# Kernel optimization log

Measured on AMD Instinct MI355X. Metric: run time of the kernel, lower is better.

## Reference

```python
import jax, jax.numpy as jnp
import numpy as np

B, S, FEAT = 64, 196, 512
D_MODEL, D_INPUT = 1024, 512
HEADS = 8          # cross-attention heads
SYNC_HEADS = 8     # neuron-sync attention heads (num_attn_heads)
ITERS = 50         # thought ticks
MEM = 25           # memory_length
NLM_H = 16         # memory_hidden_dims
OUT = 1000         # out_dims


def _n(key, i, shape, scale=0.02):
    return scale * jax.random.normal(jax.random.fold_in(key, i), shape, dtype=jnp.float32)


def setup_inputs() -> dict:
    key = jax.random.key(0)
    return {
        "x": jax.random.normal(jax.random.fold_in(key, 0), (B, S, FEAT), dtype=jnp.float32),
        "kv_w": _n(key, 1, (D_INPUT, FEAT)), "kv_b": jnp.zeros((D_INPUT,), jnp.float32),
        "ln_kv_s": jnp.ones((D_INPUT,), jnp.float32), "ln_kv_b": jnp.zeros((D_INPUT,), jnp.float32),
        "q_w": _n(key, 2, (D_INPUT, D_MODEL)), "q_b": jnp.zeros((D_INPUT,), jnp.float32),
        "in_proj_w": _n(key, 3, (3 * D_INPUT, D_INPUT)), "in_proj_b": jnp.zeros((3 * D_INPUT,), jnp.float32),
        "out_proj_w": _n(key, 4, (D_INPUT, D_INPUT)), "out_proj_b": jnp.zeros((D_INPUT,), jnp.float32),
        "W_q": _n(key, 5, (D_MODEL, D_MODEL), 0.03), "W_k": _n(key, 6, (D_MODEL, D_MODEL), 0.03),
        "W_v": _n(key, 7, (D_MODEL, D_MODEL), 0.03),
        "syn_w": _n(key, 8, (2 * D_MODEL, D_INPUT + D_MODEL)), "syn_b": jnp.zeros((2 * D_MODEL,), jnp.float32),
        "syn_ln_s": jnp.ones((D_MODEL,), jnp.float32), "syn_ln_b": jnp.zeros((D_MODEL,), jnp.float32),
        "nlm_w1": _n(key, 9, (MEM, 2 * NLM_H, D_MODEL), 0.1), "nlm_b1": jnp.zeros((D_MODEL, 2 * NLM_H), jnp.float32),
        "nlm_w2": _n(key, 10, (NLM_H, 2, D_MODEL), 0.1), "nlm_b2": jnp.zeros((D_MODEL, 2), jnp.float32),
        "start_activated_state": _n(key, 11, (D_MODEL,), 0.03),
        "start_trace": _n(key, 12, (D_MODEL, MEM), 0.03),
        "out_w": _n(key, 13, (OUT, D_MODEL)), "out_b": jnp.zeros((OUT,), jnp.float32),
    }


def _ln(x, s, b, eps=1e-5):
    m = x.mean(-1, keepdims=True)
    v = x.var(-1, keepdims=True)
    return (x - m) / jnp.sqrt(v + eps) * s + b


def _glu(x):
    a, g = jnp.split(x, 2, axis=-1)
    return a * jax.nn.sigmoid(g)


def reference(x, kv_w, kv_b, ln_kv_s, ln_kv_b, q_w, q_b, in_proj_w, in_proj_b,
              out_proj_w, out_proj_b, W_q, W_k, W_v, syn_w, syn_b, syn_ln_s, syn_ln_b,
              nlm_w1, nlm_b1, nlm_w2, nlm_b2, start_activated_state, start_trace,
              out_w, out_b):
    b = x.shape[0]
    dh_sync = D_MODEL // SYNC_HEADS
    dh = D_INPUT // HEADS

    # kv_proj: Linear + LayerNorm over backbone features (backbone='none')
    kv = _ln(x @ kv_w.T + kv_b, ln_kv_s, ln_kv_b)  # (B,S,Di)
    wq_c, wk_c, wv_c = jnp.split(in_proj_w, 3, axis=0)
    bq_c, bk_c, bv_c = jnp.split(in_proj_b, 3, axis=0)
    Kc = (kv @ wk_c.T + bk_c).reshape(b, S, HEADS, dh).transpose(0, 2, 1, 3)  # (B,H,S,dh)
    Vc = (kv @ wv_c.T + bv_c).reshape(b, S, HEADS, dh).transpose(0, 2, 1, 3)

    def sync_attn(hist, cur):
        # hist: (B,D,T) post-activation history; cur: (B,D) current post-activations
        hr = jnp.swapaxes(hist, 1, 2)  # (B,T,D)
        T = hr.shape[1]
        Q = (hr @ W_q.T).reshape(b, T, SYNC_HEADS, dh_sync).transpose(0, 2, 1, 3)  # (B,H,T,dh)
        K = (hr @ W_k.T).reshape(b, T, SYNC_HEADS, dh_sync).transpose(0, 2, 1, 3)
        V = (cur @ W_v.T).reshape(b, SYNC_HEADS, dh_sync)  # (B,H,dh)
        # neuron-vs-neuron scores: (B,H,dh,dh)
        scores = jnp.einsum('bhtd,bhte->bhde', Q, K) / jnp.sqrt(jnp.float32(dh_sync))
        w = jax.nn.softmax(scores, axis=-1)
        att = jnp.einsum('bhde,bhe->bhd', w, V)  # (B,H,dh)
        # torch: attended.transpose(1,2).reshape(B, D)
        return att.transpose(0, 2, 1).reshape(b, D_MODEL)

    def cross_attn(sync_a):
        q = sync_a @ q_w.T + q_b  # (B,Di)
        Qh = (q @ wq_c.T + bq_c).reshape(b, HEADS, 1, dh)
        s = jnp.einsum('bhqd,bhkd->bhqk', Qh, Kc) / jnp.sqrt(jnp.float32(dh))
        w = jax.nn.softmax(s, axis=-1)
        o = jnp.einsum('bhqk,bhkd->bhqd', w, Vc).transpose(0, 2, 1, 3).reshape(b, D_INPUT)
        return o @ out_proj_w.T + out_proj_b

    state_trace0 = jnp.broadcast_to(start_trace[None], (b, D_MODEL, MEM))
    act0 = jnp.broadcast_to(start_activated_state[None], (b, D_MODEL))
    hist0 = jnp.broadcast_to(start_activated_state[None, :, None], (b, D_MODEL, MEM))
    log_nc = jnp.log(jnp.float32(OUT))

    def tick(carry, _):
        st, act, hist = carry
        sync_a = sync_attn(hist, act)                     # action synchronisation
        ao = cross_attn(sync_a)                           # (B,Di)
        pre = jnp.concatenate([ao, act], axis=-1)
        state = _ln(_glu(pre @ syn_w.T + syn_b), syn_ln_s, syn_ln_b)  # synapse MLP (depth 1)
        st = jnp.concatenate([st[:, :, 1:], state[:, :, None]], axis=-1)  # sliding pre-act trace
        # per-neuron deep NLM (SuperLinear einsums)
        h = _glu(jnp.einsum('bdm,mhd->bdh', st, nlm_w1) + nlm_b1)
        act_new = _glu(jnp.einsum('bdh,hod->bdo', h, nlm_w2) + nlm_b2)[..., 0]
        hist = jnp.concatenate([hist[:, :, 1:], act_new[:, :, None]], axis=-1)
        sync_o = sync_attn(hist, act_new)                 # output synchronisation
        pred = sync_o @ out_w.T + out_b
        logp = jax.nn.log_softmax(pred, axis=-1)
        ne = -jnp.sum(jnp.exp(logp) * logp, axis=-1) / log_nc
        cert = jnp.stack([ne, 1.0 - ne], axis=-1)
        return (st, act_new, hist), (pred, cert, sync_o)

    _, (preds, certs, syncs) = jax.lax.scan(tick, (state_trace0, act0, hist0), None, length=ITERS)
    predictions = jnp.transpose(preds, (1, 2, 0))  # (B,OUT,T)
    certainties = jnp.transpose(certs, (1, 2, 0))  # (B,2,T)
    return predictions, certainties, syncs[-1]
```

## Files before the change

kernel.cpp:

```cpp
#include <hip/hip_runtime.h>
#include <hip/hip_bf16.h>

typedef __attribute__((ext_vector_type(8))) short short8v;
typedef __attribute__((ext_vector_type(4))) float f32x4;
typedef __attribute__((ext_vector_type(4))) float float4v;

#define DEV __device__ __forceinline__

DEV short f2bfs(float x){
  union { float f; unsigned u; } v; v.f = x;
  unsigned r = (v.u + 0x7FFFu + ((v.u >> 16) & 1u)) >> 16;
  return (short)(unsigned short)r;
}
DEV float bfs2f(short s){
  union { unsigned u; float f; } v; v.u = ((unsigned)(unsigned short)s) << 16;
  return v.f;
}
DEV float sigm(float x){ return 1.f / (1.f + __expf(-x)); }
DEV int zmap(int j){ int g = (j >= 1024) ? 1 : 0; int i = j - (g << 10); return (i & 15) + ((i >> 4) << 5) + (g << 4); }

struct EpiF32 {
  float* C; int ldc;
  DEV void op(const f32x4 (&acc)[4][2], int m0, int n0, int l15, int l4, const float* bias) const {
#pragma unroll
    for (int mi = 0; mi < 4; mi++)
#pragma unroll
      for (int ni = 0; ni < 2; ni++){
        int n = n0 + ni*16 + l15;
        float bb = bias ? bias[n] : 0.f;
#pragma unroll
        for (int r = 0; r < 4; r++){
          int m = m0 + mi*16 + l4*4 + r;
          C[(size_t)m*ldc + n] = acc[mi][ni][r] + bb;
        }
      }
  }
};

struct EpiBF16 {
  short* C; int ldc; int domap;
  DEV void op(const f32x4 (&acc)[4][2], int m0, int n0, int l15, int l4, const float* bias) const {
#pragma unroll
    for (int mi = 0; mi < 4; mi++)
#pragma unroll
      for (int ni = 0; ni < 2; ni++){
        int n = n0 + ni*16 + l15;
        float bb = bias ? bias[n] : 0.f;
#pragma unroll
        for (int r = 0; r < 4; r++){
          int m = m0 + mi*16 + l4*4 + r;
          int mr = domap ? zmap(m) : m;
          C[(size_t)mr*ldc + n] = f2bfs(acc[mi][ni][r] + bb);
        }
      }
  }
};

struct EpiQKV {
  short* Qb; short* Kb; float* vc; int slot;
  DEV void op(const f32x4 (&acc)[4][2], int m0, int n0, int l15, int l4, const float* bias) const {
#pragma unroll
    for (int mi = 0; mi < 4; mi++)
#pragma unroll
      for (int ni = 0; ni < 2; ni++){
        int n = n0 + ni*16 + l15;
#pragma unroll
        for (int r = 0; r < 4; r++){
          int m = m0 + mi*16 + l4*4 + r;
          float v = acc[mi][ni][r];
          if (n < 1024)       Qb[((size_t)m*1024 + n)*32 + slot] = f2bfs(v);
          else if (n < 2048)  Kb[((size_t)m*1024 + (n-1024))*32 + slot] = f2bfs(v);
          else                vc[(size_t)m*1024 + (n-2048)] = v;
        }
      }
  }
};

struct EpiPred {
  float* outp;
  DEV void op(const f32x4 (&acc)[4][2], int m0, int n0, int l15, int l4, const float* bias) const {
#pragma unroll
    for (int mi = 0; mi < 4; mi++)
#pragma unroll
      for (int ni = 0; ni < 2; ni++){
        int n = n0 + ni*16 + l15;
        if (n >= 1000) continue;
        float bb = bias[n];
#pragma unroll
        for (int r = 0; r < 4; r++){
          int m = m0 + mi*16 + l4*4 + r;
          int b = m / 50, tt = m - b*50;
          outp[(size_t)b*50000 + (size_t)n*50 + tt] = acc[mi][ni][r] + bb;
        }
      }
  }
};

struct EpiGlu {
  float* u; float* stats;
  DEV void op(const f32x4 (&acc)[4][2], int m0, int n0, int l15, int l4, const float* bias) const {
    float ba = bias[n0 + l15], bg = bias[n0 + 16 + l15];
    int i = l15 + ((n0 >> 5) << 4);
#pragma unroll
    for (int mi = 0; mi < 4; mi++)
#pragma unroll
      for (int r = 0; r < 4; r++){
        int m = m0 + mi*16 + l4*4 + r;
        float a = acc[mi][0][r] + ba;
        float g = acc[mi][1][r] + bg;
        float uv = a * sigm(g);
        u[(size_t)m*1024 + i] = uv;
        float s = uv, s2 = uv*uv;
#pragma unroll
        for (int off = 1; off < 16; off <<= 1){ s += __shfl_xor(s, off); s2 += __shfl_xor(s2, off); }
        if (l15 == 0){ atomicAdd(&stats[m], s); atomicAdd(&stats[64 + m], s2); }
      }
  }
};

struct EpiKVpre {
  short* C; float* stats;
  DEV void op(const f32x4 (&acc)[4][2], int m0, int n0, int l15, int l4, const float* bias) const {
    float b0 = bias[n0 + l15], b1 = bias[n0 + 16 + l15];
#pragma unroll
    for (int mi = 0; mi < 4; mi++)
#pragma unroll
      for (int r = 0; r < 4; r++){
        int m = m0 + mi*16 + l4*4 + r;
        float v0 = acc[mi][0][r] + b0;
        float v1 = acc[mi][1][r] + b1;
        C[(size_t)m*512 + n0 + l15]      = f2bfs(v0);
        C[(size_t)m*512 + n0 + 16 + l15] = f2bfs(v1);
        float s = v0 + v1, s2 = v0*v0 + v1*v1;
#pragma unroll
        for (int off = 1; off < 16; off <<= 1){ s += __shfl_xor(s, off); s2 += __shfl_xor(s2, off); }
        if (l15 == 0){ atomicAdd(&stats[m*2], s); atomicAdd(&stats[m*2 + 1], s2); }
      }
  }
};

template<bool ABF16, typename EPI>
__global__ __launch_bounds__(256) void gemm_tn(const void* __restrict__ Aptr, int lda,
    const short* __restrict__ Bw, int ldb, const float* __restrict__ bias,
    int K, float* zbuf, int zn, EPI epi)
{
  int tid = threadIdx.x;
  if (zbuf != nullptr && blockIdx.x == 0 && blockIdx.y == 0 && tid < zn) zbuf[tid] = 0.f;
  const int w = tid >> 6, l15 = tid & 15, l4 = (tid >> 4) & 3;
  const int m0 = blockIdx.y * 64;
  const int n0 = blockIdx.x * 128 + w * 32;
  f32x4 acc[4][2];
#pragma unroll
  for (int mi = 0; mi < 4; mi++)
#pragma unroll
    for (int ni = 0; ni < 2; ni++)
      acc[mi][ni] = (f32x4){0.f, 0.f, 0.f, 0.f};
#pragma unroll 4
  for (int kk = 0; kk < K; kk += 32){
    const int ks = kk + l4*8;
    short8v a[4], bfr[2];
#pragma unroll
    for (int mi = 0; mi < 4; mi++){
      const size_t row = (size_t)(m0 + mi*16 + l15);
      if (ABF16){
        a[mi] = *(const short8v*)((const short*)Aptr + row*lda + ks);
      } else {
        const float* ap = (const float*)Aptr + row*lda + ks;
        float4v f0 = *(const float4v*)ap;
        float4v f1 = *(const float4v*)(ap + 4);
        short8v t;
        t[0]=f2bfs(f0[0]); t[1]=f2bfs(f0[1]); t[2]=f2bfs(f0[2]); t[3]=f2bfs(f0[3]);
        t[4]=f2bfs(f1[0]); t[5]=f2bfs(f1[1]); t[6]=f2bfs(f1[2]); t[7]=f2bfs(f1[3]);
        a[mi] = t;
      }
    }
#pragma unroll
    for (int ni = 0; ni < 2; ni++)
      bfr[ni] = *(const short8v*)(Bw + (size_t)(n0 + ni*16 + l15)*ldb + ks);
#pragma unroll
    for (int mi = 0; mi < 4; mi++)
#pragma unroll
      for (int ni = 0; ni < 2; ni++)
        acc[mi][ni] = __builtin_amdgcn_mfma_f32_16x16x32_bf16(a[mi], bfr[ni], acc[mi][ni], 0, 0, 0);
  }
  epi.op(acc, m0, n0, l15, l4, bias);
}

__global__ __launch_bounds__(256) void cross_attn_k(const float* __restrict__ Qh,
    const short* __restrict__ Kc, const short* __restrict__ Vc, short* __restrict__ oa_bf)
{
  int h = blockIdx.x, b = blockIdx.y, tid = threadIdx.x;
  __shared__ float qs[64];
  __shared__ float wsm[256];
  __shared__ float red[256];
  if (tid < 64) qs[tid] = Qh[b*512 + h*64 + tid];
  __syncthreads();
  float sv = -1e30f;
  if (tid < 196){
    const short* kp = Kc + ((size_t)(b*196 + tid)*512 + h*64);
    float acc = 0.f;
#pragma unroll
    for (int j = 0; j < 64; j += 8){
      short8v kv8 = *(const short8v*)(kp + j);
#pragma unroll
      for (int u8 = 0; u8 < 8; u8++) acc += bfs2f(kv8[u8]) * qs[j + u8];
    }
    sv = acc * 0.125f;
  }
  red[tid] = sv; __syncthreads();
  for (int s = 128; s > 0; s >>= 1){ if (tid < s) red[tid] = fmaxf(red[tid], red[tid + s]); __syncthreads(); }
  float M = red[0]; __syncthreads();
  float e = (tid < 196) ? __expf(sv - M) : 0.f;
  wsm[tid] = e; red[tid] = e; __syncthreads();
  for (int s = 128; s > 0; s >>= 1){ if (tid < s) red[tid] += red[tid + s]; __syncthreads(); }
  float Z = red[0]; __syncthreads();
  int d = tid & 63, c = tid >> 6;
  float acc = 0.f;
  for (int s = c; s < 196; s += 4) acc += wsm[s] * bfs2f(Vc[(size_t)(b*196 + s)*512 + h*64 + d]);
  red[tid] = acc; __syncthreads();
  if (tid < 64){
    float o = (red[tid] + red[tid + 64] + red[tid + 128] + red[tid + 192]) / Z;
    oa_bf[(size_t)b*1536 + h*64 + tid] = f2bfs(o);
  }
}

__global__ __launch_bounds__(256) void nlm_k(const float* __restrict__ u, const float* __restrict__ stats,
    const float* __restrict__ g_s, const float* __restrict__ g_b,
    float* __restrict__ st, const float* __restrict__ w1, const float* __restrict__ b1,
    const float* __restrict__ w2, const float* __restrict__ b2, short* __restrict__ oa_bf, int t)
{
  int tid = threadIdx.x;
  int d_i = tid & 15, b_i = (tid >> 4) & 7, half = tid >> 7;
  int d = blockIdx.x*16 + d_i, b = blockIdx.y*8 + b_i;
  float mu = stats[b] * (1.f/1024.f);
  float var = stats[64 + b] * (1.f/1024.f) - mu*mu;
  float rs = rsqrtf(var + 1e-5f);
  float uv = u[b*1024 + d];
  float state = (uv - mu)*rs*g_s[d] + g_b[d];
  int slot = t % 25;
  if (half == 0) st[((size_t)b*1024 + d)*25 + slot] = state;
  float stv[25];
  int p0 = (t + 1) % 25;
#pragma unroll
  for (int m = 0; m < 25; m++){
    int p = p0 + m; if (p >= 25) p -= 25;
    stv[m] = (p == slot) ? state : st[((size_t)b*1024 + d)*25 + p];
  }
  float pre[16];
#pragma unroll
  for (int hh = 0; hh < 16; hh++) pre[hh] = b1[d*32 + half*16 + hh];
  for (int m = 0; m < 25; m++){
    float sm = stv[m];
#pragma unroll
    for (int hh = 0; hh < 16; hh++) pre[hh] += sm * w1[(size_t)(m*32 + half*16 + hh)*1024 + d];
  }
  __shared__ float pl[2][8][16][16];
#pragma unroll
  for (int hh = 0; hh < 16; hh++) pl[half][b_i][hh][d_i] = pre[hh];
  __syncthreads();
  if (half == 0){
    float p2a = b2[d*2 + 0], p2g = b2[d*2 + 1];
#pragma unroll
    for (int i = 0; i < 16; i++){
      float hv = pl[0][b_i][i][d_i] * sigm(pl[1][b_i][i][d_i]);
      p2a += hv * w2[(size_t)(i*2 + 0)*1024 + d];
      p2g += hv * w2[(size_t)(i*2 + 1)*1024 + d];
    }
    float act = p2a * sigm(p2g);
    oa_bf[(size_t)b*1536 + 512 + d] = f2bfs(act);
  }
}

__global__ __launch_bounds__(256) void sync_attn_k(const short* __restrict__ Qbuf, const short* __restrict__ Kbuf,
    const float* __restrict__ vcur, float* __restrict__ S, short* __restrict__ S_bf,
    short* __restrict__ SyncO, int t)
{
  int h = blockIdx.x, b = blockIdx.y, tid = threadIdx.x;
  __shared__ short8v qlds[512];
  __shared__ short8v klds[512];
  const short* qg = Qbuf + ((size_t)b*1024 + h*128)*32;
  const short* kg = Kbuf + ((size_t)b*1024 + h*128)*32;
#pragma unroll
  for (int it = 0; it < 2; it++){
    int ch = tid + 256*it;
    int d = ch >> 2, c = ch & 3;
    int cs = c ^ ((d >> 1) & 3);
    qlds[d*4 + cs] = *(const short8v*)(qg + d*32 + c*8);
    klds[d*4 + cs] = *(const short8v*)(kg + d*32 + c*8);
  }
  __syncthreads();
  int w = tid >> 6, l15 = tid & 15, l4 = (tid >> 4) & 3;
  short8v af[2], bfr[8];
#pragma unroll
  for (int mi2 = 0; mi2 < 2; mi2++){
    int d = (2*w + mi2)*16 + l15;
    af[mi2] = qlds[d*4 + (l4 ^ ((d >> 1) & 3))];
  }
#pragma unroll
  for (int ni = 0; ni < 8; ni++){
    int e = ni*16 + l15;
    bfr[ni] = klds[e*4 + (l4 ^ ((e >> 1) & 3))];
  }
// ... 15 lines not shown
#pragma unroll
  for (int mi2 = 0; mi2 < 2; mi2++)
#pragma unroll
    for (int r = 0; r < 4; r++){
      float sv[8]; float mx = -1e30f;
#pragma unroll
      for (int ni = 0; ni < 8; ni++){ sv[ni] = acc[mi2][ni][r]*scale; mx = fmaxf(mx, sv[ni]); }
#pragma unroll
      for (int off = 1; off < 16; off <<= 1) mx = fmaxf(mx, __shfl_xor(mx, off));
      float den = 0.f, num = 0.f;
#pragma unroll
      for (int ni = 0; ni < 8; ni++){ float p = __expf(sv[ni] - mx); den += p; num += p*Vv[ni]; }
#pragma unroll
      for (int off = 1; off < 16; off <<= 1){ den += __shfl_xor(den, off); num += __shfl_xor(num, off); }
      if (l15 == 0){
        int d = (2*w + mi2)*16 + l4*4 + r;
        float att = num / den;
        int oi = b*1024 + d*8 + h;
        S[oi] = att;
        S_bf[oi] = f2bfs(att);
        if (t >= 0) SyncO[((size_t)b*50 + t)*1024 + d*8 + h] = f2bfs(att);
      }
    }
}

__global__ __launch_bounds__(256) void vecmat_k(const float* __restrict__ W, int ldw,
    const float* __restrict__ v, const float* __restrict__ add, float* __restrict__ out, int K, int domap)
{
  int w = threadIdx.x >> 6, l = threadIdx.x & 63;
  int n = blockIdx.x*4 + w;
  float s = 0.f;
  for (int k = l; k < K; k += 64) s += W[(size_t)n*ldw + k]*v[k];
#pragma unroll
  for (int off = 32; off; off >>= 1) s += __shfl_xor(s, off);
  if (l == 0){ float o = s + (add ? add[n] : 0.f); out[domap ? zmap(n) : n] = o; }
}

__global__ void castW_k(short* dst, int dld, int drow0, int dcol0,
    const float* src, int sld, int N, int K, int transp, int domap)
{
  size_t idx = (size_t)blockIdx.x*256 + threadIdx.x;
  size_t tot = (size_t)N*K;
  if (idx >= tot) return;
  int n = idx / K, k = idx - (size_t)n*K;
  float vv = 0.f;
  if (src) vv = transp ? src[(size_t)k*sld + n] : src[(size_t)n*sld + k];
// ... 17 lines not shown
  kvp[i] = f2bfs((v - mu)*rsqrtf(var + 1e-5f)*s[c] + bb[c]);
}

__global__ void fill_k(short* Qbuf, short* Kbuf, float* vcur, short* oa_bf,
    float* st, const float* q0, const float* k0, const float* v0,
    const float* start, const float* strace)
{
  size_t i = (size_t)blockIdx.x*256 + threadIdx.x;
  const size_t R0 = 64u*1024u*32u;
  if (i < R0){
    int c = i & 31; int d = (i >> 5) & 1023;
    Qbuf[i] = (c < 25) ? f2bfs(q0[d]) : 0;
    Kbuf[i] = (c < 25) ? f2bfs(k0[d]) : 0;
    return;
  }
  i -= R0;
  if (i < 65536){
    int d = i & 1023; int b = i >> 10;
    vcur[i] = v0[d];
    oa_bf[(size_t)b*1536 + 512 + d] = f2bfs(start[d]);
    return;
  }
  i -= 65536;
  if (i < (size_t)64*1024*25){
    st[i] = strace[i % 25600];
  }
}

__global__ __launch_bounds__(256) void cert_k(const float* __restrict__ preds, float* __restrict__ cert)
{
  int t = blockIdx.x, b = blockIdx.y, tid = threadIdx.x;
  __shared__ float red[256];
  float v[4]; float mx = -1e30f;
#pragma unroll
  for (int i = 0; i < 4; i++){
    int o = tid + i*256;
    v[i] = (o < 1000) ? preds[(size_t)b*50000 + (size_t)o*50 + t] : -1e30f;
    mx = fmaxf(mx, v[i]);
  }
  red[tid] = mx; __syncthreads();
  for (int s = 128; s; s >>= 1){ if (tid < s) red[tid] = fmaxf(red[tid], red[tid + s]); __syncthreads(); }
  float M = red[0]; __syncthreads();
  float z = 0.f, wsum = 0.f;
#pragma unroll
  for (int i = 0; i < 4; i++){
    int o = tid + i*256;
    if (o < 1000){ float p = v[i] - M; float e = __expf(p); z += e; wsum += e*p; }
  }
// ... 52 lines not shown
  auto alloc = [&](size_t bytes)->char*{ char* p = ws + off; off = (off + bytes + 255) & ~(size_t)255; return p; };

  short* qw_B   = (short*)alloc((size_t)1024*512*2);
  short* opw_B  = (short*)alloc((size_t)512*512*2);
  short* Wfq    = (short*)alloc((size_t)512*1024*2);
  float* bfq    = (float*)alloc(512*4);
  short* Wz     = (short*)alloc((size_t)2048*1536*2);
  float* bz     = (float*)alloc(2048*4);
  short* Wqkv   = (short*)alloc((size_t)3072*1024*2);
  short* outwB  = (short*)alloc((size_t)1024*1024*2);
  short* kvw_B  = (short*)alloc((size_t)512*512*2);
  short* wkc_B  = (short*)alloc((size_t)512*512*2);
  short* wvc_B  = (short*)alloc((size_t)512*512*2);
  short* kvp    = (short*)alloc((size_t)12544*512*2);
  float* kvstats= (float*)alloc((size_t)25088*4);
  short* Kc     = (short*)alloc((size_t)12544*512*2);
  short* Vc     = (short*)alloc((size_t)12544*512*2);
  short* Qbuf   = (short*)alloc((size_t)64*1024*32*2);
  short* Kbuf   = (short*)alloc((size_t)64*1024*32*2);
  float* vcur   = (float*)alloc((size_t)65536*4);
  float* S      = (float*)alloc((size_t)65536*4);
  short* S_bf   = (short*)alloc((size_t)65536*2);
  short* SyncO  = (short*)alloc((size_t)64*50*1024*2);
  float* Qh     = (float*)alloc((size_t)32768*4);
  short* oa_bf  = (short*)alloc((size_t)64*1536*2);
  float* ubuf   = (float*)alloc((size_t)65536*4);
  float* stats  = (float*)alloc(128*4);
  float* st     = (float*)alloc((size_t)1638400*4);
  float* q0     = (float*)alloc(1024*4);
  float* k0     = (float*)alloc(1024*4);
  float* v0     = (float*)alloc(1024*4);
  (void)ws_size; (void)in_sizes; (void)n_in; (void)out_size;

  dim3 blk(256);

  castW_k<<<dim3((1024*512+255)/256), blk, 0, stream>>>(qw_B, 512, 0, 0, q_w, 1024, 1024, 512, 1, 0);
  castW_k<<<dim3((512*512+255)/256), blk, 0, stream>>>(opw_B, 512, 0, 0, out_proj_w, 512, 512, 512, 1, 0);
  castW_k<<<dim3((2048*1024+255)/256), blk, 0, stream>>>(Wz, 1536, 0, 512, syn_w + 512, 1536, 2048, 1024, 0, 1);
  castW_k<<<dim3((1024*1024+255)/256), blk, 0, stream>>>(Wqkv, 1024, 0, 0, W_q, 1024, 1024, 1024, 0, 0);
  castW_k<<<dim3((1024*1024+255)/256), blk, 0, stream>>>(Wqkv, 1024, 1024, 0, W_k, 1024, 1024, 1024, 0, 0);
  castW_k<<<dim3((1024*1024+255)/256), blk, 0, stream>>>(Wqkv, 1024, 2048, 0, W_v, 1024, 1024, 1024, 0, 0);
  castW_k<<<dim3((1000*1024+255)/256), blk, 0, stream>>>(outwB, 1024, 0, 0, out_w, 1024, 1000, 1024, 0, 0);
  castW_k<<<dim3((24*1024+255)/256), blk, 0, stream>>>(outwB, 1024, 1000, 0, nullptr, 0, 24, 1024, 0, 0);
  castW_k<<<dim3((512*512+255)/256), blk, 0, stream>>>(kvw_B, 512, 0, 0, kv_w, 512, 512, 512, 0, 0);
  castW_k<<<dim3((512*512+255)/256), blk, 0, stream>>>(wkc_B, 512, 0, 0, in_proj_w + 512*512, 512, 512, 512, 0, 0);
  castW_k<<<dim3((512*512+255)/256), blk, 0, stream>>>(wvc_B, 512, 0, 0, in_proj_w + 1024*512, 512, 512, 512, 0, 0);

  vecmat_k<<<dim3(256), blk, 0, stream>>>(W_q, 1024, start_act, nullptr, q0, 1024, 0);
  vecmat_k<<<dim3(256), blk, 0, stream>>>(W_k, 1024, start_act, nullptr, k0, 1024, 0);
  vecmat_k<<<dim3(256), blk, 0, stream>>>(W_v, 1024, start_act, nullptr, v0, 1024, 0);
  vecmat_k<<<dim3(128), blk, 0, stream>>>(in_proj_w, 512, q_b, in_proj_b, bfq, 512, 0);
  vecmat_k<<<dim3(512), blk, 0, stream>>>(syn_w, 1536, out_proj_b, syn_b, bz, 512, 1);

  gemm_tn<false, EpiBF16><<<dim3(8, 8), blk, 0, stream>>>(in_proj_w, 512, qw_B, 512, nullptr, 512, nullptr, 0, EpiBF16{Wfq, 1024, 0});
  gemm_tn<false, EpiBF16><<<dim3(4, 32), blk, 0, stream>>>(syn_w, 1536, opw_B, 512, nullptr, 512, nullptr, 0, EpiBF16{Wz, 1536, 1});

  zero_k<<<dim3(98), blk, 0, stream>>>(kvstats, 25088);
  gemm_tn<false, EpiKVpre><<<dim3(4, 196), blk, 0, stream>>>(x, 512, kvw_B, 512, kv_b, 512, nullptr, 0, EpiKVpre{kvp, kvstats});
  ln_inplace_k<<<dim3(25088), blk, 0, stream>>>(kvp, kvstats, ln_kv_s, ln_kv_b);
  gemm_tn<true, EpiBF16><<<dim3(4, 196), blk, 0, stream>>>(kvp, 512, wkc_B, 512, in_proj_b + 512, 512, nullptr, 0, EpiBF16{Kc, 512, 0});
  gemm_tn<true, EpiBF16><<<dim3(4, 196), blk, 0, stream>>>(kvp, 512, wvc_B, 512, in_proj_b + 1024, 512, nullptr, 0, EpiBF16{Vc, 512, 0});

  fill_k<<<dim3(14848), blk, 0, stream>>>(Qbuf, Kbuf, vcur, oa_bf, st, q0, k0, v0, start_act, strace);
  sync_attn_k<<<dim3(8, 64), blk, 0, stream>>>(Qbuf, Kbuf, vcur, S, S_bf, SyncO, -1);

  for (int t = 0; t < 50; t++){
    gemm_tn<true, EpiF32><<<dim3(4, 1), blk, 0, stream>>>(S_bf, 1024, Wfq, 1024, bfq, 1024, stats, 128, EpiF32{Qh, 512});
    cross_attn_k<<<dim3(8, 64), blk, 0, stream>>>(Qh, Kc, Vc, oa_bf);
    gemm_tn<true, EpiGlu><<<dim3(16, 1), blk, 0, stream>>>(oa_bf, 1536, Wz, 1536, bz, 1536, nullptr, 0, EpiGlu{ubuf, stats});
    nlm_k<<<dim3(64, 8), blk, 0, stream>>>(ubuf, stats, syn_ln_s, syn_ln_b, st, nlm_w1, nlm_b1, nlm_w2, nlm_b2, oa_bf, t);
    gemm_tn<true, EpiQKV><<<dim3(24, 1), blk, 0, stream>>>(oa_bf + 512, 1536, Wqkv, 1024, nullptr, 1024, nullptr, 0, EpiQKV{Qbuf, Kbuf, vcur, t % 25});
    sync_attn_k<<<dim3(8, 64), blk, 0, stream>>>(Qbuf, Kbuf, vcur, S, S_bf, SyncO, t);
  }

  gemm_tn<true, EpiPred><<<dim3(8, 50), blk, 0, stream>>>(SyncO, 1024, outwB, 1024, out_b, 1024, nullptr, 0, EpiPred{out});
  cert_k<<<dim3(50, 64), blk, 0, stream>>>(out, out + 3200000);
  copy_sync_k<<<dim3(256), blk, 0, stream>>>(S, out + 3206400);
}
```

Measured before the change: 7.639 ms.

## Fuse 50-tick recurrent loop into one persistent kernel with grid barriers

Replaces the roughly 300 per-tick kernel launches with a single persistent cooperative kernel. Its blocks loop over the phases (Q projection fused into cross-attention, GLU GEMM with split-K partials, NLM, QKV GEMM with split-K, sync attention) and separate them with a hand-written atomic grid barrier. The change also moves the state trace to a slot-major layout so NLM reads coalesce. It removes launch overhead and lets the small GEMMs spread over more blocks, at the cost of barrier latency. Correctness depends on every block being co-resident, which the grid size computed from the occupancy query is meant to guarantee.

```diff
diff --git a/kernel.cpp b/kernel.cpp
--- a/kernel.cpp
+++ b/kernel.cpp
@@ -19,181 +19,65 @@
 DEV float sigm(float x){ return 1.f / (1.f + __expf(-x)); }
 DEV int zmap(int j){ int g = (j >= 1024) ? 1 : 0; int i = j - (g << 10); return (i & 15) + ((i >> 4) << 5) + (g << 4); }
 
-struct EpiF32 {
-  float* C; int ldc;
-  DEV void op(const f32x4 (&acc)[4][2], int m0, int n0, int l15, int l4, const float* bias) const {
-#pragma unroll
-    for (int mi = 0; mi < 4; mi++)
-#pragma unroll
-      for (int ni = 0; ni < 2; ni++){
-        int n = n0 + ni*16 + l15;
-        float bb = bias ? bias[n] : 0.f;
-#pragma unroll
-        for (int r = 0; r < 4; r++){
-          int m = m0 + mi*16 + l4*4 + r;
-          C[(size_t)m*ldc + n] = acc[mi][ni][r] + bb;
-        }
-      }
-  }
-};
-
-struct EpiBF16 {
-  short* C; int ldc; int domap;
-  DEV void op(const f32x4 (&acc)[4][2], int m0, int n0, int l15, int l4, const float* bias) const {
-#pragma unroll
-    for (int mi = 0; mi < 4; mi++)
-#pragma unroll
-      for (int ni = 0; ni < 2; ni++){
-        int n = n0 + ni*16 + l15;
-        float bb = bias ? bias[n] : 0.f;
-#pragma unroll
-        for (int r = 0; r < 4; r++){
-          int m = m0 + mi*16 + l4*4 + r;
-          int mr = domap ? zmap(m) : m;
-          C[(size_t)mr*ldc + n] = f2bfs(acc[mi][ni][r] + bb);
-        }
-      }
-  }
-};
-
-struct EpiQKV {
-  short* Qb; short* Kb; float* vc; int slot;
-  DEV void op(const f32x4 (&acc)[4][2], int m0, int n0, int l15, int l4, const float* bias) const {
-#pragma unroll
-    for (int mi = 0; mi < 4; mi++)
-#pragma unroll
-      for (int ni = 0; ni < 2; ni++){
-        int n = n0 + ni*16 + l15;
-#pragma unroll
-        for (int r = 0; r < 4; r++){
-          int m = m0 + mi*16 + l4*4 + r;
-          float v = acc[mi][ni][r];
-          if (n < 1024)       Qb[((size_t)m*1024 + n)*32 + slot] = f2bfs(v);
-          else if (n < 2048)  Kb[((size_t)m*1024 + (n-1024))*32 + slot] = f2bfs(v);
-          else                vc[(size_t)m*1024 + (n-2048)] = v;
-        }
-      }
-  }
-};
-
-struct EpiPred {
-  float* outp;
-  DEV void op(const f32x4 (&acc)[4][2], int m0, int n0, int l15, int l4, const float* bias) const {
-#pragma unroll
-    for (int mi = 0; mi < 4; mi++)
-#pragma unroll
-      for (int ni = 0; ni < 2; ni++){
-        int n = n0 + ni*16 + l15;
-        if (n >= 1000) continue;
-        float bb = bias[n];
-#pragma unroll
-        for (int r = 0; r < 4; r++){
-          int m = m0 + mi*16 + l4*4 + r;
-          int b = m / 50, tt = m - b*50;
-          outp[(size_t)b*50000 + (size_t)n*50 + tt] = acc[mi][ni][r] + bb;
-        }
-      }
-  }
-};
-
-struct EpiGlu {
-  float* u; float* stats;
-  DEV void op(const f32x4 (&acc)[4][2], int m0, int n0, int l15, int l4, const float* bias) const {
-    float ba = bias[n0 + l15], bg = bias[n0 + 16 + l15];
-    int i = l15 + ((n0 >> 5) << 4);
-#pragma unroll
-    for (int mi = 0; mi < 4; mi++)
-#pragma unroll
-      for (int r = 0; r < 4; r++){
-        int m = m0 + mi*16 + l4*4 + r;
-        float a = acc[mi][0][r] + ba;
-        float g = acc[mi][1][r] + bg;
-        float uv = a * sigm(g);
-        u[(size_t)m*1024 + i] = uv;
-        float s = uv, s2 = uv*uv;
-#pragma unroll
-        for (int off = 1; off < 16; off <<= 1){ s += __shfl_xor(s, off); s2 += __shfl_xor(s2, off); }
-        if (l15 == 0){ atomicAdd(&stats[m], s); atomicAdd(&stats[64 + m], s2); }
-      }
-  }
-};
-
-struct EpiKVpre {
-  short* C; float* stats;
-  DEV void op(const f32x4 (&acc)[4][2], int m0, int n0, int l15, int l4, const float* bias) const {
-    float b0 = bias[n0 + l15], b1 = bias[n0 + 16 + l15];
-#pragma unroll
-    for (int mi = 0; mi < 4; mi++)
-#pragma unroll
-      for (int r = 0; r < 4; r++){
-        int m = m0 + mi*16 + l4*4 + r;
-        float v0 = acc[mi][0][r] + b0;
-        float v1 = acc[mi][1][r] + b1;
-        C[(size_t)m*512 + n0 + l15]      = f2bfs(v0);
-        C[(size_t)m*512 + n0 + 16 + l15] = f2bfs(v1);
-        float s = v0 + v1, s2 = v0*v0 + v1*v1;
-#pragma unroll
-        for (int off = 1; off < 16; off <<= 1){ s += __shfl_xor(s, off); s2 += __shfl_xor(s2, off); }
-        if (l15 == 0){ atomicAdd(&stats[m*2], s); atomicAdd(&stats[m*2 + 1], s2); }
-      }
-  }
-};
-
-template<bool ABF16, typename EPI>
-__global__ __launch_bounds__(256) void gemm_tn(const void* __restrict__ Aptr, int lda,
-    const short* __restrict__ Bw, int ldb, const float* __restrict__ bias,
-    int K, float* zbuf, int zn, EPI epi)
-{
-  int tid = threadIdx.x;
-  if (zbuf != nullptr && blockIdx.x == 0 && blockIdx.y == 0 && tid < zn) zbuf[tid] = 0.f;
-  const int w = tid >> 6, l15 = tid & 15, l4 = (tid >> 4) & 3;
-  const int m0 = blockIdx.y * 64;
-  const int n0 = blockIdx.x * 128 + w * 32;
-  f32x4 acc[4][2];
-#pragma unroll
-  for (int mi = 0; mi < 4; mi++)
-#pragma unroll
-    for (int ni = 0; ni < 2; ni++)
-      acc[mi][ni] = (f32x4){0.f, 0.f, 0.f, 0.f};
+DEV void gbar(unsigned* bar, int nb){
+  __syncthreads();
+  if (threadIdx.x == 0){
+    __builtin_amdgcn_fence(__ATOMIC_RELEASE, "agent");
+    unsigned* gen = bar + 128;
+    unsigned g = __hip_atomic_load(gen, __ATOMIC_RELAXED, __HIP_MEMORY_SCOPE_AGENT);
+    int lane = blockIdx.x & 7;
+    __hip_atomic_fetch_add(bar + lane*16, 1u, __ATOMIC_RELAXED, __HIP_MEMORY_SCOPE_AGENT);
+    if (blockIdx.x == 0){
+      unsigned sum;
+      do {
+        sum = 0;
+#pragma unroll
+        for (int i = 0; i < 8; i++) sum += __hip_atomic_load(bar + i*16, __ATOMIC_RELAXED, __HIP_MEMORY_SCOPE_AGENT);
+      } while (sum < (unsigned)nb);
+#pragma unroll
+      for (int i = 0; i < 8; i++) __hip_atomic_store(bar + i*16, 0u, __ATOMIC_RELAXED, __HIP_MEMORY_SCOPE_AGENT);
+      __hip_atomic_store(gen, g + 1u, __ATOMIC_RELEASE, __HIP_MEMORY_SCOPE_AGENT);
+    } else {
+      while (__hip_atomic_load(gen, __ATOMIC_RELAXED, __HIP_MEMORY_SCOPE_AGENT) == g)
+        __builtin_amdgcn_s_sleep(1);
+    }
+    __builtin_amdgcn_fence(__ATOMIC_ACQUIRE, "agent");
+  }
+  __syncthreads();
+  __builtin_amdgcn_fence(__ATOMIC_ACQUIRE, "agent");
+}
+
+
+DEV void phase_qhcross(int u, const short* __restrict__ Wfq, const float* __restrict__ bfq,
+    const short* __restrict__ Kc, const short* __restrict__ Vc, const short* __restrict__ S_bf,
+    short* __restrict__ oa_bf, float* __restrict__ stats, float* smf, int tid, int zero_stats)
+{
+  float* Srow = smf;
+  float* qs   = smf + 1024;
+  float* wsm  = smf + 1088;
+  float* red  = smf + 1344;
+  int h = u & 7, b = u >> 3;
+  __syncthreads();
+  const short* sp = S_bf + b*1024;
+#pragma unroll
+  for (int r = 0; r < 4; r++){ int idx = tid + r*256; Srow[idx] = bfs2f(sp[idx]); }
+  if (zero_stats && tid < 128) stats[tid] = 0.f;
+  __syncthreads();
+  {
+    int d = tid & 63, c = tid >> 6;
+    const short* wp = Wfq + (size_t)(h*64 + d)*1024 + c*256;
+    const float* srp = Srow + c*256;
+    float acc = 0.f;
 #pragma unroll 4
-  for (int kk = 0; kk < K; kk += 32){
-    const int ks = kk + l4*8;
-    short8v a[4], bfr[2];
-#pragma unroll
-    for (int mi = 0; mi < 4; mi++){
-      const size_t row = (size_t)(m0 + mi*16 + l15);
-      if (ABF16){
-        a[mi] = *(const short8v*)((const short*)Aptr + row*lda + ks);
-      } else {
-        const float* ap = (const float*)Aptr + row*lda + ks;
-        float4v f0 = *(const float4v*)ap;
-        float4v f1 = *(const float4v*)(ap + 4);
-        short8v t;
-        t[0]=f2bfs(f0[0]); t[1]=f2bfs(f0[1]); t[2]=f2bfs(f0[2]); t[3]=f2bfs(f0[3]);
-        t[4]=f2bfs(f1[0]); t[5]=f2bfs(f1[1]); t[6]=f2bfs(f1[2]); t[7]=f2bfs(f1[3]);
-        a[mi] = t;
-      }
+    for (int i = 0; i < 256; i += 8){
+      short8v wv = *(const short8v*)(wp + i);
+#pragma unroll
+      for (int j = 0; j < 8; j++) acc += bfs2f(wv[j]) * srp[i + j];
     }
-#pragma unroll
-    for (int ni = 0; ni < 2; ni++)
-      bfr[ni] = *(const short8v*)(Bw + (size_t)(n0 + ni*16 + l15)*ldb + ks);
-#pragma unroll
-    for (int mi = 0; mi < 4; mi++)
-#pragma unroll
-      for (int ni = 0; ni < 2; ni++)
-        acc[mi][ni] = __builtin_amdgcn_mfma_f32_16x16x32_bf16(a[mi], bfr[ni], acc[mi][ni], 0, 0, 0);
-  }
-  epi.op(acc, m0, n0, l15, l4, bias);
-}
-
-__global__ __launch_bounds__(256) void cross_attn_k(const float* __restrict__ Qh,
-    const short* __restrict__ Kc, const short* __restrict__ Vc, short* __restrict__ oa_bf)
-{
-  int h = blockIdx.x, b = blockIdx.y, tid = threadIdx.x;
-  __shared__ float qs[64];
-  __shared__ float wsm[256];
-  __shared__ float red[256];
-  if (tid < 64) qs[tid] = Qh[b*512 + h*64 + tid];
+    red[tid] = acc;
+  }
+  __syncthreads();
+  if (tid < 64) qs[tid] = bfq[h*64 + tid] + red[tid] + red[tid+64] + red[tid+128] + red[tid+192];
   __syncthreads();
   float sv = -1e30f;
   if (tid < 196){
@@ -208,76 +92,183 @@
     sv = acc * 0.125f;
   }
   red[tid] = sv; __syncthreads();
-  for (int s = 128; s > 0; s >>= 1){ if (tid < s) red[tid] = fmaxf(red[tid], red[tid + s]); __syncthreads(); }
+  for (int s = 128; s > 0; s >>= 1){ if (tid < s) red[tid] = fmaxf(red[tid], red[tid+s]); __syncthreads(); }
   float M = red[0]; __syncthreads();
   float e = (tid < 196) ? __expf(sv - M) : 0.f;
   wsm[tid] = e; red[tid] = e; __syncthreads();
-  for (int s = 128; s > 0; s >>= 1){ if (tid < s) red[tid] += red[tid + s]; __syncthreads(); }
+  for (int s = 128; s > 0; s >>= 1){ if (tid < s) red[tid] += red[tid+s]; __syncthreads(); }
   float Z = red[0]; __syncthreads();
-  int d = tid & 63, c = tid >> 6;
+  int dd = tid & 63, cc = tid >> 6;
   float acc = 0.f;
-  for (int s = c; s < 196; s += 4) acc += wsm[s] * bfs2f(Vc[(size_t)(b*196 + s)*512 + h*64 + d]);
+  for (int s = cc; s < 196; s += 4) acc += wsm[s] * bfs2f(Vc[(size_t)(b*196 + s)*512 + h*64 + dd]);
   red[tid] = acc; __syncthreads();
   if (tid < 64){
-    float o = (red[tid] + red[tid + 64] + red[tid + 128] + red[tid + 192]) / Z;
+    float o = (red[tid] + red[tid+64] + red[tid+128] + red[tid+192]) / Z;
     oa_bf[(size_t)b*1536 + h*64 + tid] = f2bfs(o);
   }
-}
-
-__global__ __launch_bounds__(256) void nlm_k(const float* __restrict__ u, const float* __restrict__ stats,
-    const float* __restrict__ g_s, const float* __restrict__ g_b,
-    float* __restrict__ st, const float* __restrict__ w1, const float* __restrict__ b1,
-    const float* __restrict__ w2, const float* __restrict__ b2, short* __restrict__ oa_bf, int t)
-{
-  int tid = threadIdx.x;
+  __syncthreads();
+}
+
+DEV void phase_glu(int u, const short* __restrict__ Wz, const float* __restrict__ bz,
+    const short* __restrict__ oa_bf, float* __restrict__ ubuf, float* __restrict__ stats,
+    float* smf, int tid)
+{
+  float* part   = smf;
+  float* statsl = smf + 8192;
+  int n0 = u * 32;
+  __syncthreads();
+  if (tid < 128) statsl[tid] = 0.f;
+  int w = tid >> 6, l15 = tid & 15, l4 = (tid >> 4) & 3;
+  f32x4 acc[4][2];
+#pragma unroll
+  for (int mi = 0; mi < 4; mi++)
+#pragma unroll
+    for (int ni = 0; ni < 2; ni++) acc[mi][ni] = (f32x4){0.f,0.f,0.f,0.f};
+#pragma unroll 2
+  for (int it = 0; it < 12; it++){
+    int ks = w*384 + it*32 + l4*8;
+    short8v a4[4], bb[2];
+#pragma unroll
+    for (int mi = 0; mi < 4; mi++)
+      a4[mi] = *(const short8v*)(oa_bf + (size_t)(mi*16 + l15)*1536 + ks);
+#pragma unroll
+    for (int ni = 0; ni < 2; ni++)
+      bb[ni] = *(const short8v*)(Wz + (size_t)(n0 + ni*16 + l15)*1536 + ks);
+#pragma unroll
+    for (int mi = 0; mi < 4; mi++)
+#pragma unroll
+      for (int ni = 0; ni < 2; ni++)
+        acc[mi][ni] = __builtin_amdgcn_mfma_f32_16x16x32_bf16(a4[mi], bb[ni], acc[mi][ni], 0, 0, 0);
+  }
+#pragma unroll
+  for (int mi = 0; mi < 4; mi++)
+#pragma unroll
+    for (int ni = 0; ni < 2; ni++)
+#pragma unroll
+      for (int r = 0; r < 4; r++)
+        part[w*2048 + (mi*16 + l4*4 + r)*32 + ni*16 + l15] = acc[mi][ni][r];
+  __syncthreads();
+  int m = tid >> 2;
+  float s1 = 0.f, s2 = 0.f;
+#pragma unroll
+  for (int e = 0; e < 4; e++){
+    int j = ((tid & 3) << 2) + e;
+    float a = part[m*32 + j] + part[2048 + m*32 + j] + part[4096 + m*32 + j] + part[6144 + m*32 + j] + bz[n0 + j];
+    float g = part[m*32 + 16 + j] + part[2048 + m*32 + 16 + j] + part[4096 + m*32 + 16 + j] + part[6144 + m*32 + 16 + j] + bz[n0 + 16 + j];
+    float uv = a * sigm(g);
+    ubuf[(size_t)m*1024 + (n0 >> 1) + j] = uv;
+    s1 += uv; s2 += uv*uv;
+  }
+  atomicAdd(&statsl[m], s1); atomicAdd(&statsl[64 + m], s2);
+  __syncthreads();
+  if (tid < 64){ atomicAdd(&stats[tid], statsl[tid]); atomicAdd(&stats[64 + tid], statsl[64 + tid]); }
+  __syncthreads();
+}
+
+DEV void phase_nlm(int u, const float* __restrict__ ubuf, const float* __restrict__ stats,
+    const float* __restrict__ g_s, const float* __restrict__ g_b, float* __restrict__ st,
+    const float* __restrict__ w1, const float* __restrict__ b1,
+    const float* __restrict__ w2, const float* __restrict__ b2,
+    short* __restrict__ oa_bf, int t, float* smf, int tid)
+{
+  float* pl = smf;
+  int x = u & 63, y = u >> 6;
   int d_i = tid & 15, b_i = (tid >> 4) & 7, half = tid >> 7;
-  int d = blockIdx.x*16 + d_i, b = blockIdx.y*8 + b_i;
+  int d = x*16 + d_i, b = y*8 + b_i;
   float mu = stats[b] * (1.f/1024.f);
   float var = stats[64 + b] * (1.f/1024.f) - mu*mu;
   float rs = rsqrtf(var + 1e-5f);
-  float uv = u[b*1024 + d];
+  float uv = ubuf[b*1024 + d];
   float state = (uv - mu)*rs*g_s[d] + g_b[d];
   int slot = t % 25;
-  if (half == 0) st[((size_t)b*1024 + d)*25 + slot] = state;
-  float stv[25];
+  if (half == 0) st[(size_t)slot*65536 + b*1024 + d] = state;
+  float pre[16];
+#pragma unroll
+  for (int hh = 0; hh < 16; hh++) pre[hh] = b1[d*32 + half*16 + hh];
   int p0 = (t + 1) % 25;
-#pragma unroll
+#pragma unroll 5
   for (int m = 0; m < 25; m++){
     int p = p0 + m; if (p >= 25) p -= 25;
-    stv[m] = (p == slot) ? state : st[((size_t)b*1024 + d)*25 + p];
-  }
-  float pre[16];
-#pragma unroll
-  for (int hh = 0; hh < 16; hh++) pre[hh] = b1[d*32 + half*16 + hh];
-  for (int m = 0; m < 25; m++){
-    float sm = stv[m];
+    float sm = (p == slot) ? state : st[(size_t)p*65536 + b*1024 + d];
 #pragma unroll
     for (int hh = 0; hh < 16; hh++) pre[hh] += sm * w1[(size_t)(m*32 + half*16 + hh)*1024 + d];
   }
-  __shared__ float pl[2][8][16][16];
-#pragma unroll
-  for (int hh = 0; hh < 16; hh++) pl[half][b_i][hh][d_i] = pre[hh];
+  __syncthreads();
+#pragma unroll
+  for (int hh = 0; hh < 16; hh++) pl[((half*8 + b_i)*16 + hh)*16 + d_i] = pre[hh];
   __syncthreads();
   if (half == 0){
     float p2a = b2[d*2 + 0], p2g = b2[d*2 + 1];
 #pragma unroll
     for (int i = 0; i < 16; i++){
-      float hv = pl[0][b_i][i][d_i] * sigm(pl[1][b_i][i][d_i]);
+      float hv = pl[((b_i)*16 + i)*16 + d_i] * sigm(pl[((8 + b_i)*16 + i)*16 + d_i]);
       p2a += hv * w2[(size_t)(i*2 + 0)*1024 + d];
       p2g += hv * w2[(size_t)(i*2 + 1)*1024 + d];
     }
     float act = p2a * sigm(p2g);
     oa_bf[(size_t)b*1536 + 512 + d] = f2bfs(act);
   }
-}
-
-__global__ __launch_bounds__(256) void sync_attn_k(const short* __restrict__ Qbuf, const short* __restrict__ Kbuf,
+  __syncthreads();
+}
+
+DEV void phase_qkv(int u, const short* __restrict__ Wqkv, const short* __restrict__ act_bf,
+    short* __restrict__ Qb, short* __restrict__ Kb, float* __restrict__ vc, int slot,
+    float* smf, int tid)
+{
+  float* part = smf;
+  int n0 = u * 32;
+  __syncthreads();
+  int w = tid >> 6, l15 = tid & 15, l4 = (tid >> 4) & 3;
+  f32x4 acc[4][2];
+#pragma unroll
+  for (int mi = 0; mi < 4; mi++)
+#pragma unroll
+    for (int ni = 0; ni < 2; ni++) acc[mi][ni] = (f32x4){0.f,0.f,0.f,0.f};
+#pragma unroll 2
+  for (int it = 0; it < 8; it++){
+    int ks = w*256 + it*32 + l4*8;
+    short8v a4[4], bb[2];
+#pragma unroll
+    for (int mi = 0; mi < 4; mi++)
+      a4[mi] = *(const short8v*)(act_bf + (size_t)(mi*16 + l15)*1536 + ks);
+#pragma unroll
+    for (int ni = 0; ni < 2; ni++)
+      bb[ni] = *(const short8v*)(Wqkv + (size_t)(n0 + ni*16 + l15)*1024 + ks);
+#pragma unroll
+    for (int mi = 0; mi < 4; mi++)
+#pragma unroll
+      for (int ni = 0; ni < 2; ni++)
+        acc[mi][ni] = __builtin_amdgcn_mfma_f32_16x16x32_bf16(a4[mi], bb[ni], acc[mi][ni], 0, 0, 0);
+  }
+#pragma unroll
+  for (int mi = 0; mi < 4; mi++)
+#pragma unroll
+    for (int ni = 0; ni < 2; ni++)
+#pragma unroll
+      for (int r = 0; r < 4; r++)
+        part[w*2048 + (mi*16 + l4*4 + r)*32 + ni*16 + l15] = acc[mi][ni][r];
+  __syncthreads();
+  int m = tid >> 2;
+#pragma unroll
+  for (int e = 0; e < 8; e++){
+    int nl = ((tid & 3) << 3) + e;
+    float v = part[m*32 + nl] + part[2048 + m*32 + nl] + part[4096 + m*32 + nl] + part[6144 + m*32 + nl];
+    int n = n0 + nl;
+    if (n < 1024)      Qb[((size_t)m*1024 + n)*32 + slot] = f2bfs(v);
+    else if (n < 2048) Kb[((size_t)m*1024 + (n-1024))*32 + slot] = f2bfs(v);
+    else               vc[(size_t)m*1024 + (n-2048)] = v;
+  }
+  __syncthreads();
+}
+
+DEV void phase_sync(int u, int t, const short* __restrict__ Qbuf, const short* __restrict__ Kbuf,
     const float* __restrict__ vcur, float* __restrict__ S, short* __restrict__ S_bf,
-    short* __restrict__ SyncO, int t)
-{
-  int h = blockIdx.x, b = blockIdx.y, tid = threadIdx.x;
-  __shared__ short8v qlds[512];
-  __shared__ short8v klds[512];
+    short* __restrict__ SyncO, float* smf, int tid)
+{
+  short8v* qlds = (short8v*)smf;
+  short8v* klds = ((short8v*)smf) + 512;
+  int h = u & 7, b = u >> 3;
+  __syncthreads();
   const short* qg = Qbuf + ((size_t)b*1024 + h*128)*32;
   const short* kg = Kbuf + ((size_t)b*1024 + h*128)*32;
 #pragma unroll
@@ -339,6 +330,155 @@
         if (t >= 0) SyncO[((size_t)b*50 + t)*1024 + d*8 + h] = f2bfs(att);
       }
     }
+  __syncthreads();
+}
+
+__global__ __launch_bounds__(256, 2) void tick_all_k(
+    const short* __restrict__ Wfq, const float* __restrict__ bfq,
+    const short* __restrict__ Kc, const short* __restrict__ Vc,
+    const short* __restrict__ Wz, const float* __restrict__ bz,
+    float* __restrict__ ubuf, float* __restrict__ stats,
+    const float* __restrict__ g_s, const float* __restrict__ g_b,
+    float* __restrict__ st,
+    const float* __restrict__ w1, const float* __restrict__ b1,
+    const float* __restrict__ w2, const float* __restrict__ b2,
+    const short* __restrict__ Wqkv,
+    short* __restrict__ Qbuf, short* __restrict__ Kbuf, float* __restrict__ vcur,
+    float* __restrict__ S, short* __restrict__ S_bf, short* __restrict__ SyncO,
+    short* __restrict__ oa_bf, unsigned* bar)
+{
+  __shared__ float smf[8320];
+  const int tid = threadIdx.x;
+  const int bid = blockIdx.x;
+  const int nb  = gridDim.x;
+
+  for (int u = bid; u < 512; u += nb) phase_sync(u, -1, Qbuf, Kbuf, vcur, S, S_bf, SyncO, smf, tid);
+  gbar(bar, nb);
+
+#pragma unroll 1
+  for (int t = 0; t < 50; t++){
+    for (int u = bid; u < 512; u += nb)
+      phase_qhcross(u, Wfq, bfq, Kc, Vc, S_bf, oa_bf, stats, smf, tid, u == 0);
+    gbar(bar, nb);
+    for (int u = bid; u < 64; u += nb)
+      phase_glu(u, Wz, bz, oa_bf, ubuf, stats, smf, tid);
+    gbar(bar, nb);
+    for (int u = bid; u < 512; u += nb)
+      phase_nlm(u, ubuf, stats, g_s, g_b, st, w1, b1, w2, b2, oa_bf, t, smf, tid);
+    gbar(bar, nb);
+    for (int u = bid; u < 96; u += nb)
+      phase_qkv(u, Wqkv, oa_bf + 512, Qbuf, Kbuf, vcur, t % 25, smf, tid);
+    gbar(bar, nb);
+    for (int u = bid; u < 512; u += nb)
+      phase_sync(u, t, Qbuf, Kbuf, vcur, S, S_bf, SyncO, smf, tid);
+    gbar(bar, nb);
+  }
+}
+
+struct EpiBF16 {
+  short* C; int ldc; int domap;
+  DEV void op(const f32x4 (&acc)[4][2], int m0, int n0, int l15, int l4, const float* bias) const {
+#pragma unroll
+    for (int mi = 0; mi < 4; mi++)
+#pragma unroll
+      for (int ni = 0; ni < 2; ni++){
+        int n = n0 + ni*16 + l15;
+        float bb = bias ? bias[n] : 0.f;
+#pragma unroll
+        for (int r = 0; r < 4; r++){
+          int m = m0 + mi*16 + l4*4 + r;
+          int mr = domap ? zmap(m) : m;
+          C[(size_t)mr*ldc + n] = f2bfs(acc[mi][ni][r] + bb);
+        }
+      }
+  }
+};
+
+struct EpiPred {
+  float* outp;
+  DEV void op(const f32x4 (&acc)[4][2], int m0, int n0, int l15, int l4, const float* bias) const {
+#pragma unroll
+    for (int mi = 0; mi < 4; mi++)
+#pragma unroll
+      for (int ni = 0; ni < 2; ni++){
+        int n = n0 + ni*16 + l15;
+        if (n >= 1000) continue;
+        float bb = bias[n];
+#pragma unroll
+        for (int r = 0; r < 4; r++){
+          int m = m0 + mi*16 + l4*4 + r;
+          int b = m / 50, tt = m - b*50;
+          outp[(size_t)b*50000 + (size_t)n*50 + tt] = acc[mi][ni][r] + bb;
+        }
+      }
+  }
+};
+
+struct EpiKVpre {
+  short* C; float* stats;
+  DEV void op(const f32x4 (&acc)[4][2], int m0, int n0, int l15, int l4, const float* bias) const {
+    float b0 = bias[n0 + l15], b1 = bias[n0 + 16 + l15];
+#pragma unroll
+    for (int mi = 0; mi < 4; mi++)
+#pragma unroll
+      for (int r = 0; r < 4; r++){
+        int m = m0 + mi*16 + l4*4 + r;
+        float v0 = acc[mi][0][r] + b0;
+        float v1 = acc[mi][1][r] + b1;
+        C[(size_t)m*512 + n0 + l15]      = f2bfs(v0);
+        C[(size_t)m*512 + n0 + 16 + l15] = f2bfs(v1);
+        float s = v0 + v1, s2 = v0*v0 + v1*v1;
+#pragma unroll
+        for (int off = 1; off < 16; off <<= 1){ s += __shfl_xor(s, off); s2 += __shfl_xor(s2, off); }
+        if (l15 == 0){ atomicAdd(&stats[m*2], s); atomicAdd(&stats[m*2 + 1], s2); }
+      }
+  }
+};
+
+template<bool ABF16, typename EPI>
+__global__ __launch_bounds__(256) void gemm_tn(const void* __restrict__ Aptr, int lda,
+    const short* __restrict__ Bw, int ldb, const float* __restrict__ bias,
+    int K, EPI epi)
+{
+  int tid = threadIdx.x;
+  const int w = tid >> 6, l15 = tid & 15, l4 = (tid >> 4) & 3;
+  const int m0 = blockIdx.y * 64;
+  const int n0 = blockIdx.x * 128 + w * 32;
+  f32x4 acc[4][2];
+#pragma unroll
+  for (int mi = 0; mi < 4; mi++)
+#pragma unroll
+    for (int ni = 0; ni < 2; ni++)
+      acc[mi][ni] = (f32x4){0.f, 0.f, 0.f, 0.f};
+#pragma unroll 4
+  for (int kk = 0; kk < K; kk += 32){
+    const int ks = kk + l4*8;
+    short8v a[4], bfr[2];
+#pragma unroll
+    for (int mi = 0; mi < 4; mi++){
+      const size_t row = (size_t)(m0 + mi*16 + l15);
+      if (ABF16){
+        a[mi] = *(const short8v*)((const short*)Aptr + row*lda + ks);
+      } else {
+        const float* ap = (const float*)Aptr + row*lda + ks;
+        float4v f0 = *(const float4v*)ap;
+        float4v f1 = *(const float4v*)(ap + 4);
+        short8v tt;
+        tt[0]=f2bfs(f0[0]); tt[1]=f2bfs(f0[1]); tt[2]=f2bfs(f0[2]); tt[3]=f2bfs(f0[3]);
+        tt[4]=f2bfs(f1[0]); tt[5]=f2bfs(f1[1]); tt[6]=f2bfs(f1[2]); tt[7]=f2bfs(f1[3]);
+        a[mi] = tt;
+      }
+    }
+#pragma unroll
+    for (int ni = 0; ni < 2; ni++)
+      bfr[ni] = *(const short8v*)(Bw + (size_t)(n0 + ni*16 + l15)*ldb + ks);
+#pragma unroll
+    for (int mi = 0; mi < 4; mi++)
+#pragma unroll
+      for (int ni = 0; ni < 2; ni++)
+        acc[mi][ni] = __builtin_amdgcn_mfma_f32_16x16x32_bf16(a[mi], bfr[ni], acc[mi][ni], 0, 0, 0);
+  }
+  epi.op(acc, m0, n0, l15, l4, bias);
 }
 
 __global__ __launch_bounds__(256) void vecmat_k(const float* __restrict__ W, int ldw,
@@ -402,8 +542,9 @@
     return;
   }
   i -= 65536;
-  if (i < (size_t)64*1024*25){
-    st[i] = strace[i % 25600];
+  if (i < (size_t)25*65536){
+    int p = (int)(i >> 16); int rem = (int)(i & 65535); int d = rem & 1023;
+    st[i] = strace[d*25 + p];
   }
 }
 
@@ -502,7 +643,6 @@
   float* S      = (float*)alloc((size_t)65536*4);
   short* S_bf   = (short*)alloc((size_t)65536*2);
   short* SyncO  = (short*)alloc((size_t)64*50*1024*2);
-  float* Qh     = (float*)alloc((size_t)32768*4);
   short* oa_bf  = (short*)alloc((size_t)64*1536*2);
   float* ubuf   = (float*)alloc((size_t)65536*4);
   float* stats  = (float*)alloc(128*4);
@@ -510,10 +650,12 @@
   float* q0     = (float*)alloc(1024*4);
   float* k0     = (float*)alloc(1024*4);
   float* v0     = (float*)alloc(1024*4);
+  unsigned* bar = (unsigned*)alloc(1024);
   (void)ws_size; (void)in_sizes; (void)n_in; (void)out_size;
 
   dim3 blk(256);
 
+  zero_k<<<dim3(1), blk, 0, stream>>>((float*)bar, 256);
   castW_k<<<dim3((1024*512+255)/256), blk, 0, stream>>>(qw_B, 512, 0, 0, q_w, 1024, 1024, 512, 1, 0);
   castW_k<<<dim3((512*512+255)/256), blk, 0, stream>>>(opw_B, 512, 0, 0, out_proj_w, 512, 512, 512, 1, 0);
   castW_k<<<dim3((2048*1024+255)/256), blk, 0, stream>>>(Wz, 1536, 0, 512, syn_w + 512, 1536, 2048, 1024, 0, 1);
@@ -532,28 +674,33 @@
   vecmat_k<<<dim3(128), blk, 0, stream>>>(in_proj_w, 512, q_b, in_proj_b, bfq, 512, 0);
   vecmat_k<<<dim3(512), blk, 0, stream>>>(syn_w, 1536, out_proj_b, syn_b, bz, 512, 1);
 
-  gemm_tn<false, EpiBF16><<<dim3(8, 8), blk, 0, stream>>>(in_proj_w, 512, qw_B, 512, nullptr, 512, nullptr, 0, EpiBF16{Wfq, 1024, 0});
-  gemm_tn<false, EpiBF16><<<dim3(4, 32), blk, 0, stream>>>(syn_w, 1536, opw_B, 512, nullptr, 512, nullptr, 0, EpiBF16{Wz, 1536, 1});
+  gemm_tn<false, EpiBF16><<<dim3(8, 8), blk, 0, stream>>>(in_proj_w, 512, qw_B, 512, nullptr, 512, EpiBF16{Wfq, 1024, 0});
+  gemm_tn<false, EpiBF16><<<dim3(4, 32), blk, 0, stream>>>(syn_w, 1536, opw_B, 512, nullptr, 512, EpiBF16{Wz, 1536, 1});
 
   zero_k<<<dim3(98), blk, 0, stream>>>(kvstats, 25088);
-  gemm_tn<false, EpiKVpre><<<dim3(4, 196), blk, 0, stream>>>(x, 512, kvw_B, 512, kv_b, 512, nullptr, 0, EpiKVpre{kvp, kvstats});
+  gemm_tn<false, EpiKVpre><<<dim3(4, 196), blk, 0, stream>>>(x, 512, kvw_B, 512, kv_b, 512, EpiKVpre{kvp, kvstats});
   ln_inplace_k<<<dim3(25088), blk, 0, stream>>>(kvp, kvstats, ln_kv_s, ln_kv_b);
-  gemm_tn<true, EpiBF16><<<dim3(4, 196), blk, 0, stream>>>(kvp, 512, wkc_B, 512, in_proj_b + 512, 512, nullptr, 0, EpiBF16{Kc, 512, 0});
-  gemm_tn<true, EpiBF16><<<dim3(4, 196), blk, 0, stream>>>(kvp, 512, wvc_B, 512, in_proj_b + 1024, 512, nullptr, 0, EpiBF16{Vc, 512, 0});
+  gemm_tn<true, EpiBF16><<<dim3(4, 196), blk, 0, stream>>>(kvp, 512, wkc_B, 512, in_proj_b + 512, 512, EpiBF16{Kc, 512, 0});
+  gemm_tn<true, EpiBF16><<<dim3(4, 196), blk, 0, stream>>>(kvp, 512, wvc_B, 512, in_proj_b + 1024, 512, EpiBF16{Vc, 512, 0});
 
   fill_k<<<dim3(14848), blk, 0, stream>>>(Qbuf, Kbuf, vcur, oa_bf, st, q0, k0, v0, start_act, strace);
-  sync_attn_k<<<dim3(8, 64), blk, 0, stream>>>(Qbuf, Kbuf, vcur, S, S_bf, SyncO, -1);
-
-  for (int t = 0; t < 50; t++){
-    gemm_tn<true, EpiF32><<<dim3(4, 1), blk, 0, stream>>>(S_bf, 1024, Wfq, 1024, bfq, 1024, stats, 128, EpiF32{Qh, 512});
-    cross_attn_k<<<dim3(8, 64), blk, 0, stream>>>(Qh, Kc, Vc, oa_bf);
-    gemm_tn<true, EpiGlu><<<dim3(16, 1), blk, 0, stream>>>(oa_bf, 1536, Wz, 1536, bz, 1536, nullptr, 0, EpiGlu{ubuf, stats});
-    nlm_k<<<dim3(64, 8), blk, 0, stream>>>(ubuf, stats, syn_ln_s, syn_ln_b, st, nlm_w1, nlm_b1, nlm_w2, nlm_b2, oa_bf, t);
-    gemm_tn<true, EpiQKV><<<dim3(24, 1), blk, 0, stream>>>(oa_bf + 512, 1536, Wqkv, 1024, nullptr, 1024, nullptr, 0, EpiQKV{Qbuf, Kbuf, vcur, t % 25});
-    sync_attn_k<<<dim3(8, 64), blk, 0, stream>>>(Qbuf, Kbuf, vcur, S, S_bf, SyncO, t);
-  }
-
-  gemm_tn<true, EpiPred><<<dim3(8, 50), blk, 0, stream>>>(SyncO, 1024, outwB, 1024, out_b, 1024, nullptr, 0, EpiPred{out});
+
+  int nb = 256;
+  {
+    int mb = 0;
+    if (hipOccupancyMaxActiveBlocksPerMultiprocessor(&mb, reinterpret_cast<const void*>(tick_all_k), 256, 0) == hipSuccess && mb >= 1){
+      int dev = 0; hipGetDevice(&dev);
+      int ncu = 0;
+      if (hipDeviceGetAttribute(&ncu, hipDeviceAttributeMultiprocessorCount, dev) != hipSuccess || ncu <= 0) ncu = 256;
+      long cap = (long)mb * (long)ncu;
+      nb = (int)(cap < 512 ? cap : 512);
+    }
+  }
+  tick_all_k<<<dim3(nb), blk, 0, stream>>>(Wfq, bfq, Kc, Vc, Wz, bz, ubuf, stats,
+      syn_ln_s, syn_ln_b, st, nlm_w1, nlm_b1, nlm_w2, nlm_b2, Wqkv,
+      Qbuf, Kbuf, vcur, S, S_bf, SyncO, oa_bf, bar);
+
+  gemm_tn<true, EpiPred><<<dim3(8, 50), blk, 0, stream>>>(SyncO, 1024, outwB, 1024, out_b, 1024, EpiPred{out});
   cert_k<<<dim3(50, 64), blk, 0, stream>>>(out, out + 3200000);
   copy_sync_k<<<dim3(256), blk, 0, stream>>>(S, out + 3206400);
 }
```

New measurement: 9.653 ms. +26.4%, slower.
